# Optimization experiments

Measured on AMD Instinct MI355X. Metric: run time of the kernel, lower is better.

## Reference

```python
import jax, jax.numpy as jnp
import numpy as np

H = 512
S = 65  # 64 board cells + appended constant 1


def _heads(y, wk, wq, wv):
    # y: [H, S]; wk/wq/wv: [3, H, H] -> atts: [3, S, H]
    def one(wk_i, wq_i, wv_i):
        k = wk_i @ y            # [H, S]
        q = wq_i @ y            # [H, S]
        v = wv_i @ y            # [H, S]
        sm = jax.nn.softmax(k.T @ q, axis=1)  # [S, S], softmax over dim=1
        return sm @ v.T         # [S, H]
    return jax.vmap(one)(wk, wq, wv)


def setup_inputs() -> dict:
    key = jax.random.key(0)
    ks = jax.random.split(key, 10)
    r = lambda k, s: jax.random.normal(k, s, dtype=jnp.float32)
    return {
        "inputs": r(ks[0], (1, 64)),
        "embedding": r(ks[1], (H, S)),
        "wq": r(ks[2], (3, 3, H, H)),
        "wk": r(ks[3], (3, 3, H, H)),
        "wv": r(ks[4], (3, 3, H, H)),
        "linear1": r(ks[5], (3 * H, H)),
        "linear2": r(ks[6], (3 * H, H)),
        "linear3": r(ks[7], (3 * H, 2 * H)),
        "linear4": r(ks[8], (2 * H, H)),
        "linear5": r(ks[9], (H, 64)),
    }


def reference(inputs, embedding, wq, wk, wv, linear1, linear2, linear3, linear4, linear5):
    x = jnp.concatenate([inputs[0], jnp.ones((1,), inputs.dtype)])  # [S]
    y = embedding * x  # [H, S] (broadcast over rows)

    # Layer 1 (3 heads)
    a1 = _heads(y, wk[0], wq[0], wv[0])  # [3, S, H]
    y = jax.nn.relu(jnp.concatenate([a1[0], a1[1], a1[2]], axis=1) @ linear1).T  # [H, S]

    # Layer 2 -- NOTE: original code cats att11, att12, att23 (a bug we preserve)
    a2 = _heads(y, wk[1], wq[1], wv[1])
    y = jax.nn.relu(jnp.concatenate([a1[0], a1[1], a2[2]], axis=1) @ linear2).T  # [H, S]

    # Layer 3 -- NOTE: original code cats att11, att12, att33 (preserved)
    a3 = _heads(y, wk[2], wq[2], wv[2])
    y = jax.nn.relu(jnp.concatenate([a1[0], a1[1], a3[2]], axis=1) @ linear3)[64]  # [2H]

    # dropout p=0.1 -> identity in eval mode
    y = jnp.tanh(y @ linear4)  # [H]
    score = y @ linear5        # [64]
    return score[None, :]      # [1, 64]
```

## Files before the change

kernel.cpp:

```cpp
#include <hip/hip_runtime.h>
#include <hip/hip_bf16.h>
#include <math.h>

#define H 512
#define S 65
#define SP 80
#define HS (H * S)
#define PHS (H * SP)
#define KS3 24
#define KS4 16


__global__ void scale_embed_kernel(const float* __restrict__ inp,
                                   const float* __restrict__ emb,
                                   float* __restrict__ yT) {
    int i = blockIdx.x * blockDim.x + threadIdx.x;
    if (i < PHS) {
        int s = i / H;
        int h = i % H;
        float v = 0.f;
        if (s < S) {
            float x = (s == 64) ? 1.0f : inp[s];
            v = emb[h * S + s] * x;
        }
        yT[i] = v;
    }
}

__global__ void __launch_bounds__(256, 2)
kqv_gemm_tiled(const float* __restrict__ wq,
               const float* __restrict__ wk,
               const float* __restrict__ wv,
               int layer, int head0,
               const float* __restrict__ yT,
               float* __restrict__ part) {
    int slot  = blockIdx.z;
    int which = blockIdx.y;
    int mat = layer * 3 + head0 + slot;
    const float* W = (which == 0 ? wk : (which == 1 ? wq : wv)) + (size_t)mat * H * H;

    int n0   = (blockIdx.x & 7) * 64;
    int kidx = blockIdx.x >> 3;

    __shared__ float Wt[64 * 64];
    __shared__ float As[SP * 64];

    int t  = threadIdx.x;
    int nq = t & 15;
    int g  = t >> 4;

    float4 acc[5];
#pragma unroll
    for (int r = 0; r < 5; ++r) acc[r] = make_float4(0.f, 0.f, 0.f, 0.f);

    for (int ch = 0; ch < 4; ++ch) {
        int kc0 = kidx * 256 + ch * 64;
#pragma unroll
        for (int c = 0; c < 4; ++c) {
            int f = c * 256 + t;
            int wn  = f >> 4;
            int kf4 = f & 15;
            float4 w4 = *(const float4*)(W + (size_t)(n0 + wn) * H + kc0 + 4 * kf4);
            int sw = ((wn >> 2) ^ (kf4 & 7));
            int base = (4 * kf4) * 64 + 4 * sw + (wn & 3);
            Wt[base      ] = w4.x;
            Wt[base +  64] = w4.y;
            Wt[base + 128] = w4.z;
            Wt[base + 192] = w4.w;
        }
#pragma unroll
        for (int c = 0; c < 5; ++c) {
            int f = c * 256 + t;
            int as  = f >> 4;
            int kf4 = f & 15;
            *(float4*)(&As[as * 64 + 4 * kf4]) =
                *(const float4*)(yT + (size_t)as * H + kc0 + 4 * kf4);
        }
        __syncthreads();

#pragma unroll
        for (int k4 = 0; k4 < 16; ++k4) {
            int swc = 4 * (nq ^ (k4 & 7));
            float4 w0 = *(const float4*)(&Wt[(4 * k4 + 0) * 64 + swc]);
            float4 w1 = *(const float4*)(&Wt[(4 * k4 + 1) * 64 + swc]);
            float4 w2 = *(const float4*)(&Wt[(4 * k4 + 2) * 64 + swc]);
            float4 w3 = *(const float4*)(&Wt[(4 * k4 + 3) * 64 + swc]);
#pragma unroll
            for (int r = 0; r < 5; ++r) {
                float4 a = *(const float4*)(&As[(g + 16 * r) * 64 + 4 * k4]);
                acc[r].x = fmaf(a.x, w0.x, acc[r].x);
                acc[r].y = fmaf(a.x, w0.y, acc[r].y);
                acc[r].z = fmaf(a.x, w0.z, acc[r].z);
                acc[r].w = fmaf(a.x, w0.w, acc[r].w);
                acc[r].x = fmaf(a.y, w1.x, acc[r].x);
                acc[r].y = fmaf(a.y, w1.y, acc[r].y);
                acc[r].z = fmaf(a.y, w1.z, acc[r].z);
                acc[r].w = fmaf(a.y, w1.w, acc[r].w);
                acc[r].x = fmaf(a.z, w2.x, acc[r].x);
                acc[r].y = fmaf(a.z, w2.y, acc[r].y);
                acc[r].z = fmaf(a.z, w2.z, acc[r].z);
                acc[r].w = fmaf(a.z, w2.w, acc[r].w);
                acc[r].x = fmaf(a.w, w3.x, acc[r].x);
                acc[r].y = fmaf(a.w, w3.y, acc[r].y);
                acc[r].z = fmaf(a.w, w3.z, acc[r].z);
                acc[r].w = fmaf(a.w, w3.w, acc[r].w);
            }
        }
        __syncthreads();
    }

    float* P = part + (size_t)((slot * 3 + which) * 2 + kidx) * PHS;
#pragma unroll
    for (int r = 0; r < 5; ++r) {
        *(float4*)(P + (size_t)(g + 16 * r) * H + n0 + 4 * nq) = acc[r];
    }
}

__device__ __forceinline__ float score_part(const float* __restrict__ Q0,
                                            const float* __restrict__ Q1,
                                            const float* __restrict__ ka,
                                            int b, int t) {
    const float4* q0 = (const float4*)(Q0 + (size_t)b * H) + t * 32;
    const float4* q1 = (const float4*)(Q1 + (size_t)b * H) + t * 32;
    const float4* kl = (const float4*)ka + t * 32;
    float4 c0 = {0,0,0,0}, c1 = {0,0,0,0};
#pragma unroll
    for (int u = 0; u < 32; u += 2) {
        float4 qa = q0[u], qb = q1[u], k0 = kl[u];
        float4 qc = q0[u+1], qd = q1[u+1], k1 = kl[u+1];
        c0.x = fmaf(k0.x, qa.x + qb.x, c0.x);
        c0.y = fmaf(k0.y, qa.y + qb.y, c0.y);
        c0.z = fmaf(k0.z, qa.z + qb.z, c0.z);
        c0.w = fmaf(k0.w, qa.w + qb.w, c0.w);
        c1.x = fmaf(k1.x, qc.x + qd.x, c1.x);
        c1.y = fmaf(k1.y, qc.y + qd.y, c1.y);
        c1.z = fmaf(k1.z, qc.z + qd.z, c1.z);
        c1.w = fmaf(k1.w, qc.w + qd.w, c1.w);
    }
    return ((c0.x + c0.y) + (c0.z + c0.w)) + ((c1.x + c1.y) + (c1.z + c1.w));
}

__global__ void attn_kernel(const float* __restrict__ kqvp,
                            float* __restrict__ att) {
    int a = blockIdx.x;
    int slot = blockIdx.y;
    int tid = threadIdx.x;

    const float* base = kqvp + (size_t)slot * 6 * PHS;
    const float* K0 = base;
    const float* K1 = base + PHS;
    const float* Q0 = base + 2 * (size_t)PHS;
    const float* Q1 = base + 3 * (size_t)PHS;
    const float* V0 = base + 4 * (size_t)PHS;
    const float* V1 = base + 5 * (size_t)PHS;
    float* ao = att + (size_t)slot * PHS + (size_t)a * H;

    __shared__ float ka[H];
    __shared__ float sp[4 * 65];
    __shared__ float smv[S];
    __shared__ float p[S];

    ka[tid]       = K0[(size_t)a * H + tid]       + K1[(size_t)a * H + tid];
    ka[tid + 256] = K0[(size_t)a * H + tid + 256] + K1[(size_t)a * H + tid + 256];
    __syncthreads();

    {
        int b = tid & 63;
        int t = tid >> 6;
        sp[t * 65 + b] = score_part(Q0, Q1, ka, b, t);
        if (tid < 4) sp[tid * 65 + 64] = score_part(Q0, Q1, ka, 64, tid);
    }
    __syncthreads();

    if (tid < S) {
        smv[tid] = (sp[tid] + sp[65 + tid]) + (sp[130 + tid] + sp[195 + tid]);
    }
    __syncthreads();

    float maxv = -INFINITY;
    for (int i = 0; i < S; ++i) maxv = fmaxf(maxv, smv[i]);
    float sum = 0.0f;
    for (int i = 0; i < S; ++i) sum += expf(smv[i] - maxv);
    float inv = 1.0f / sum;
    if (tid < S) p[tid] = expf(smv[tid] - maxv) * inv;
    __syncthreads();

#pragma unroll
    for (int rep = 0; rep < 2; ++rep) {
        int hh = tid + rep * 256;
        float a0 = 0.f, a1 = 0.f;
#pragma unroll 4
        for (int b = 0; b < 64; b += 2) {
            a0 = fmaf(p[b    ], V0[(size_t)(b    ) * H + hh] + V1[(size_t)(b    ) * H + hh], a0);
            a1 = fmaf(p[b + 1], V0[(size_t)(b + 1) * H + hh] + V1[(size_t)(b + 1) * H + hh], a1);
        }
        a0 = fmaf(p[64], V0[(size_t)64 * H + hh] + V1[(size_t)64 * H + hh], a0);
        ao[hh] = a0 + a1;
    }
}

__device__ __forceinline__ void lin_gemm_dev(const float* __restrict__ A01,
                                             const float* __restrict__ A2,
                                             const float* __restrict__ L,
                                             float* __restrict__ Pbase,
                                             int ntile, int kidx, int kbase,
                                             int tid,
                                             float* __restrict__ Bs,
                                             float* __restrict__ As) {
    int n0 = ntile * 64;
    int nq = tid & 15;
    int g  = tid >> 4;

    float4 acc[5];
#pragma unroll
    for (int r = 0; r < 5; ++r) acc[r] = make_float4(0.f, 0.f, 0.f, 0.f);

#pragma unroll
    for (int ch = 0; ch < 2; ++ch) {
        int kg = kbase + kidx * 128 + ch * 64;
        int head = kg >> 9;
        const float* Asrc = (head < 2) ? (A01 + (size_t)head * PHS) : A2;
        int col0 = kg & 511;

#pragma unroll
        for (int c = 0; c < 4; ++c) {
            int f = c * 256 + tid;
            int kk  = f >> 4;
            int hf4 = f & 15;
            *(float4*)(&Bs[kk * 64 + 4 * hf4]) =
                *(const float4*)(L + (size_t)(kg + kk) * H + n0 + 4 * hf4);
        }
#pragma unroll
        for (int c = 0; c < 5; ++c) {
            int f = c * 256 + tid;
            int as  = f >> 4;
            int kf4 = f & 15;
            *(float4*)(&As[as * 68 + 4 * kf4]) =
                *(const float4*)(Asrc + (size_t)as * H + col0 + 4 * kf4);
        }
        __syncthreads();

#pragma unroll
        for (int k4 = 0; k4 < 16; ++k4) {
            float4 w0 = *(const float4*)(&Bs[(4 * k4 + 0) * 64 + 4 * nq]);
            float4 w1 = *(const float4*)(&Bs[(4 * k4 + 1) * 64 + 4 * nq]);
            float4 w2 = *(const float4*)(&Bs[(4 * k4 + 2) * 64 + 4 * nq]);
            float4 w3 = *(const float4*)(&Bs[(4 * k4 + 3) * 64 + 4 * nq]);
#pragma unroll
            for (int r = 0; r < 5; ++r) {
                float4 a = *(const float4*)(&As[(g + 16 * r) * 68 + 4 * k4]);
                acc[r].x = fmaf(a.x, w0.x, acc[r].x);
                acc[r].y = fmaf(a.x, w0.y, acc[r].y);
                acc[r].z = fmaf(a.x, w0.z, acc[r].z);
                acc[r].w = fmaf(a.x, w0.w, acc[r].w);
                acc[r].x = fmaf(a.y, w1.x, acc[r].x);
                acc[r].y = fmaf(a.y, w1.y, acc[r].y);
                acc[r].z = fmaf(a.y, w1.z, acc[r].z);
                acc[r].w = fmaf(a.y, w1.w, acc[r].w);
                acc[r].x = fmaf(a.z, w2.x, acc[r].x);
                acc[r].y = fmaf(a.z, w2.y, acc[r].y);
                acc[r].z = fmaf(a.z, w2.z, acc[r].z);
                acc[r].w = fmaf(a.z, w2.w, acc[r].w);
                acc[r].x = fmaf(a.w, w3.x, acc[r].x);
                acc[r].y = fmaf(a.w, w3.y, acc[r].y);
                acc[r].z = fmaf(a.w, w3.z, acc[r].z);
                acc[r].w = fmaf(a.w, w3.w, acc[r].w);
            }
        }
        __syncthreads();
    }

    float* P = Pbase + (size_t)kidx * PHS;
#pragma unroll
    for (int r = 0; r < 5; ++r) {
        *(float4*)(P + (size_t)(g + 16 * r) * H + n0 + 4 * nq) = acc[r];
    }
}

__global__ void __launch_bounds__(256, 1)
lin1plus_kernel(const float* __restrict__ att1,
                const float* __restrict__ lin1,
                const float* __restrict__ lin3,
                float* __restrict__ plin1,
                float* __restrict__ tpart) {
    __shared__ float Bs[64 * 64];
    __shared__ float As[SP * 68];
    int bx = blockIdx.x;
    int tid = threadIdx.x;

    if (bx < 96) {
        lin_gemm_dev(att1, att1 + 2 * (size_t)PHS, lin1, plin1,
                     bx & 7, bx >> 3, 0, tid, Bs, As);
    } else {
        int idx = bx - 96;
        int j2 = (idx & 3) * 256 + tid;
        int ks = idx >> 2;
        const float* row = att1 + (size_t)(ks >> 3) * PHS + (size_t)64 * H;
        int j0 = (ks & 7) * 64;
        int jbase = ks * 64;
        float a0 = 0.f, a1 = 0.f, a2 = 0.f, a3 = 0.f;
        for (int j = 0; j < 64; j += 4) {
            a0 = fmaf(row[j0 + j + 0], lin3[(size_t)(jbase + j + 0) * 1024 + j2], a0);
            a1 = fmaf(row[j0 + j + 1], lin3[(size_t)(jbase + j + 1) * 1024 + j2], a1);
            a2 = fmaf(row[j0 + j + 2], lin3[(size_t)(jbase + j + 2) * 1024 + j2], a2);
            a3 = fmaf(row[j0 + j + 3], lin3[(size_t)(jbase + j + 3) * 1024 + j2], a3);
        }
        tpart[ks * 1024 + j2] = (a0 + a1) + (a2 + a3);
    }
}

__global__ void __launch_bounds__(256, 1)
lin2ab_kernel(const float* __restrict__ att1,
              const float* __restrict__ lin2,
              float* __restrict__ plin2) {
    __shared__ float Bs[64 * 64];
    __shared__ float As[SP * 68];
    int bx = blockIdx.x;
    lin_gemm_dev(att1, att1, lin2, plin2, bx & 7, bx >> 3, 0,
                 threadIdx.x, Bs, As);
}

__global__ void __launch_bounds__(256, 1)
lin2c_kernel(const float* __restrict__ att2,
             const float* __restrict__ lin2,
             float* __restrict__ plin2) {
    __shared__ float Bs[64 * 64];
    __shared__ float As[SP * 68];
    int bx = blockIdx.x;
    lin_gemm_dev(att2, att2, lin2, plin2 + 8 * (size_t)PHS,
                 bx & 7, bx >> 3, 1024, threadIdx.x, Bs, As);
}

__global__ void combine12_relu_kernel(const float* __restrict__ part,
                                      float* __restrict__ yT) {
    int i = blockIdx.x * 256 + threadIdx.x;
    float s = 0.f;
#pragma unroll
    for (int p = 0; p < 12; ++p) s += part[(size_t)p * PHS + i];
    yT[i] = fmaxf(s, 0.0f);
}

__global__ void attn3_lin3c_kernel(const float* __restrict__ kqvp,
                                   const float* __restrict__ lin3,
                                   float* __restrict__ tpart) {
    int tid = threadIdx.x;
    int ks  = 16 + blockIdx.y;
    int j2  = blockIdx.x * 256 + tid;
    int j0  = (ks & 7) * 64;

    const float* K0 = kqvp;
    const float* K1 = kqvp + PHS;
    const float* Q0 = kqvp + 2 * (size_t)PHS;
    const float* Q1 = kqvp + 3 * (size_t)PHS;
    const float* V0 = kqvp + 4 * (size_t)PHS;
    const float* V1 = kqvp + 5 * (size_t)PHS;

    __shared__ float ka[H];
    __shared__ float sp[4 * 65];
    __shared__ float smv[S];
    __shared__ float p[S];
    __shared__ float att_s[64];

    ka[tid]       = K0[(size_t)64 * H + tid]       + K1[(size_t)64 * H + tid];
    ka[tid + 256] = K0[(size_t)64 * H + tid + 256] + K1[(size_t)64 * H + tid + 256];
    __syncthreads();

    {
        int b = tid & 63;
        int t = tid >> 6;
        sp[t * 65 + b] = score_part(Q0, Q1, ka, b, t);
        if (tid < 4) sp[tid * 65 + 64] = score_part(Q0, Q1, ka, 64, tid);
    }
    __syncthreads();

    if (tid < S) {
        smv[tid] = (sp[tid] + sp[65 + tid]) + (sp[130 + tid] + sp[195 + tid]);
    }
    __syncthreads();

    float maxv = -INFINITY;
    for (int i = 0; i < S; ++i) maxv = fmaxf(maxv, smv[i]);
    float sum = 0.0f;
    for (int i = 0; i < S; ++i) sum += expf(smv[i] - maxv);
    float inv = 1.0f / sum;
    if (tid < S) p[tid] = expf(smv[tid] - maxv) * inv;
    __syncthreads();

    if (tid < 64) {
        int hh = j0 + tid;
        float a0 = 0.f, a1 = 0.f;
#pragma unroll 4
        for (int b = 0; b < 64; b += 2) {
            a0 = fmaf(p[b    ], V0[(size_t)(b    ) * H + hh] + V1[(size_t)(b    ) * H + hh], a0);
            a1 = fmaf(p[b + 1], V0[(size_t)(b + 1) * H + hh] + V1[(size_t)(b + 1) * H + hh], a1);
        }
        a0 = fmaf(p[64], V0[(size_t)64 * H + hh] + V1[(size_t)64 * H + hh], a0);
        att_s[tid] = a0 + a1;
    }
    __syncthreads();

    int jbase = ks * 64;
    float a0 = 0.f, a1 = 0.f, a2 = 0.f, a3 = 0.f;
    for (int j = 0; j < 64; j += 4) {
        a0 = fmaf(att_s[j + 0], lin3[(size_t)(jbase + j + 0) * 1024 + j2], a0);
        a1 = fmaf(att_s[j + 1], lin3[(size_t)(jbase + j + 1) * 1024 + j2], a1);
        a2 = fmaf(att_s[j + 2], lin3[(size_t)(jbase + j + 2) * 1024 + j2], a2);
        a3 = fmaf(att_s[j + 3], lin3[(size_t)(jbase + j + 3) * 1024 + j2], a3);
    }
    tpart[ks * 1024 + j2] = (a0 + a1) + (a2 + a3);
}

__global__ void lin4_partial_kernel(const float* __restrict__ tpart,
                                    const float* __restrict__ lin4,
                                    float* __restrict__ upart) {
    __shared__ float tl[64];
    int hh = blockIdx.x * 256 + threadIdx.x;
    int ks = blockIdx.y;
    int j2base = ks * 64;

    if (threadIdx.x < 64) {
        int j2 = j2base + threadIdx.x;
        float s = 0.f;
#pragma unroll
        for (int p = 0; p < KS3; ++p) s += tpart[p * 1024 + j2];
        tl[threadIdx.x] = fmaxf(s, 0.f);
    }
    __syncthreads();

    float a0 = 0.f, a1 = 0.f, a2 = 0.f, a3 = 0.f;
    for (int j = 0; j < 64; j += 4) {
        a0 = fmaf(tl[j + 0], lin4[(size_t)(j2base + j + 0) * H + hh], a0);
        a1 = fmaf(tl[j + 1], lin4[(size_t)(j2base + j + 1) * H + hh], a1);
        a2 = fmaf(tl[j + 2], lin4[(size_t)(j2base + j + 2) * H + hh], a2);
        a3 = fmaf(tl[j + 3], lin4[(size_t)(j2base + j + 3) * H + hh], a3);
    }
    upart[ks * H + hh] = (a0 + a1) + (a2 + a3);
}

__global__ void final_out_kernel(const float* __restrict__ upart,
                                 const float* __restrict__ lin5,
                                 float* __restrict__ out) {
    __shared__ float u[H];
    __shared__ float pr[8][64];
    int tid = threadIdx.x;

    {
        float s = 0.f;
#pragma unroll
        for (int p = 0; p < KS4; ++p) s += upart[p * H + tid];
        u[tid] = tanhf(s);
    }
    __syncthreads();

    int o  = tid & 63;
    int sl = tid >> 6;
    float acc = 0.f;
    int h0 = sl * 64;
#pragma unroll 8
    for (int j = 0; j < 64; ++j) {
        acc = fmaf(u[h0 + j], lin5[(h0 + j) * 64 + o], acc);
    }
    pr[sl][o] = acc;
    __syncthreads();

    if (tid < 64) {
        float s = 0.f;
#pragma unroll
        for (int p = 0; p < 8; ++p) s += pr[p][tid];
        out[tid] = s;
    }
}

extern "C" void kernel_launch(void* const* d_in, const int* in_sizes, int n_in,
                              void* d_out, int out_size, void* d_ws, size_t ws_size,
                              hipStream_t stream) {
    const float* inputs  = (const float*)d_in[0];
    const float* emb     = (const float*)d_in[1];
    const float* wq      = (const float*)d_in[2];
    const float* wk      = (const float*)d_in[3];
    const float* wv      = (const float*)d_in[4];
    const float* linear1 = (const float*)d_in[5];
    const float* linear2 = (const float*)d_in[6];
    const float* linear3 = (const float*)d_in[7];
    const float* linear4 = (const float*)d_in[8];
    const float* linear5 = (const float*)d_in[9];
    float* out = (float*)d_out;

    float* ws    = (float*)d_ws;
    float* y     = ws;
    float* kqvp  = y     + PHS;
    float* att1  = kqvp  + 18 * PHS;
    float* att2  = att1  + 3 * PHS;
    float* plin1 = att2  + PHS;
    float* plin2 = plin1 + 12 * PHS;
    float* tpart = plin2 + 12 * PHS;
    float* upart = tpart + KS3 * 1024;

    const int nb  = HS / 256;
    const int nbp = PHS / 256;

    scale_embed_kernel<<<nbp, 256, 0, stream>>>(inputs, emb, y);

    kqv_gemm_tiled<<<dim3(16, 3, 3), 256, 0, stream>>>(wq, wk, wv, 0, 0, y, kqvp);
    attn_kernel<<<dim3(S, 3), 256, 0, stream>>>(kqvp, att1);
    lin1plus_kernel<<<160, 256, 0, stream>>>(att1, linear1, linear3, plin1, tpart);
    lin2ab_kernel<<<64, 256, 0, stream>>>(att1, linear2, plin2);
    combine12_relu_kernel<<<nb, 256, 0, stream>>>(plin1, y);

    kqv_gemm_tiled<<<dim3(16, 3, 1), 256, 0, stream>>>(wq, wk, wv, 1, 2, y, kqvp);
    attn_kernel<<<dim3(S, 1), 256, 0, stream>>>(kqvp, att2);
    lin2c_kernel<<<32, 256, 0, stream>>>(att2, linear2, plin2);
    combine12_relu_kernel<<<nb, 256, 0, stream>>>(plin2, y);

    kqv_gemm_tiled<<<dim3(16, 3, 1), 256, 0, stream>>>(wq, wk, wv, 2, 2, y, kqvp);
    attn3_lin3c_kernel<<<dim3(4, 8), 256, 0, stream>>>(kqvp, linear3, tpart);

    lin4_partial_kernel<<<dim3(2, KS4), 256, 0, stream>>>(tpart, linear4, upart);
    final_out_kernel<<<1, 512, 0, stream>>>(upart, linear5, out);
}
```

Baseline: 304.6 us.

## Fuse partial-sum combine and ReLU into QKV loads; merge linear kernels

The two linear-layer GEMM launches are merged into one large kernel, and the tiled shared-memory GEMM is replaced by a simple per-output dot product with 256-wide K splits, which gives 6 partials instead of 12. The separate combine-plus-ReLU kernels are removed: the templated QKV GEMM now sums the 6 partials and applies ReLU while it loads its activations. This cuts launch count and intermediate traffic. The cost is that the untiled dot product gives up shared-memory reuse, so every weight element is re-read from cache once per sequence row, and the QKV kernel's occupancy hint drops to one block.

```diff
diff --git a/kernel.cpp b/kernel.cpp
--- a/kernel.cpp
+++ b/kernel.cpp
@@ -27,16 +27,17 @@
     }
 }
 
-__global__ void __launch_bounds__(256, 2)
+template <int COMBINE>
+__global__ void __launch_bounds__(256, 1)
 kqv_gemm_tiled(const float* __restrict__ wq,
                const float* __restrict__ wk,
                const float* __restrict__ wv,
-               int layer, int head0,
-               const float* __restrict__ yT,
+               int mat0,
+               const float* __restrict__ src,
                float* __restrict__ part) {
     int slot  = blockIdx.z;
     int which = blockIdx.y;
-    int mat = layer * 3 + head0 + slot;
+    int mat = mat0 + slot;
     const float* W = (which == 0 ? wk : (which == 1 ? wq : wv)) + (size_t)mat * H * H;
 
     int n0   = (blockIdx.x & 7) * 64;
@@ -73,8 +74,21 @@
             int f = c * 256 + t;
             int as  = f >> 4;
             int kf4 = f & 15;
-            *(float4*)(&As[as * 64 + 4 * kf4]) =
-                *(const float4*)(yT + (size_t)as * H + kc0 + 4 * kf4);
+            const float* addr = src + (size_t)as * H + kc0 + 4 * kf4;
+            float4 v;
+            if (COMBINE) {
+                v = make_float4(0.f, 0.f, 0.f, 0.f);
+#pragma unroll
+                for (int p = 0; p < 6; ++p) {
+                    float4 u = *(const float4*)(addr + (size_t)p * PHS);
+                    v.x += u.x; v.y += u.y; v.z += u.z; v.w += u.w;
+                }
+                v.x = fmaxf(v.x, 0.f); v.y = fmaxf(v.y, 0.f);
+                v.z = fmaxf(v.z, 0.f); v.w = fmaxf(v.w, 0.f);
+            } else {
+                v = *(const float4*)addr;
+            }
+            *(float4*)(&As[as * 64 + 4 * kf4]) = v;
         }
         __syncthreads();
 
@@ -199,100 +213,48 @@
     }
 }
 
-__device__ __forceinline__ void lin_gemm_dev(const float* __restrict__ A01,
-                                             const float* __restrict__ A2,
-                                             const float* __restrict__ L,
-                                             float* __restrict__ Pbase,
-                                             int ntile, int kidx, int kbase,
-                                             int tid,
-                                             float* __restrict__ Bs,
-                                             float* __restrict__ As) {
-    int n0 = ntile * 64;
-    int nq = tid & 15;
-    int g  = tid >> 4;
-
-    float4 acc[5];
-#pragma unroll
-    for (int r = 0; r < 5; ++r) acc[r] = make_float4(0.f, 0.f, 0.f, 0.f);
-
-#pragma unroll
-    for (int ch = 0; ch < 2; ++ch) {
-        int kg = kbase + kidx * 128 + ch * 64;
-        int head = kg >> 9;
-        const float* Asrc = (head < 2) ? (A01 + (size_t)head * PHS) : A2;
-        int col0 = kg & 511;
-
-#pragma unroll
-        for (int c = 0; c < 4; ++c) {
-            int f = c * 256 + tid;
-            int kk  = f >> 4;
-            int hf4 = f & 15;
-            *(float4*)(&Bs[kk * 64 + 4 * hf4]) =
-                *(const float4*)(L + (size_t)(kg + kk) * H + n0 + 4 * hf4);
-        }
-#pragma unroll
-        for (int c = 0; c < 5; ++c) {
-            int f = c * 256 + tid;
-            int as  = f >> 4;
-            int kf4 = f & 15;
-            *(float4*)(&As[as * 68 + 4 * kf4]) =
-                *(const float4*)(Asrc + (size_t)as * H + col0 + 4 * kf4);
-        }
-        __syncthreads();
-
-#pragma unroll
-        for (int k4 = 0; k4 < 16; ++k4) {
-            float4 w0 = *(const float4*)(&Bs[(4 * k4 + 0) * 64 + 4 * nq]);
-            float4 w1 = *(const float4*)(&Bs[(4 * k4 + 1) * 64 + 4 * nq]);
-            float4 w2 = *(const float4*)(&Bs[(4 * k4 + 2) * 64 + 4 * nq]);
-            float4 w3 = *(const float4*)(&Bs[(4 * k4 + 3) * 64 + 4 * nq]);
-#pragma unroll
-            for (int r = 0; r < 5; ++r) {
-                float4 a = *(const float4*)(&As[(g + 16 * r) * 68 + 4 * k4]);
-                acc[r].x = fmaf(a.x, w0.x, acc[r].x);
-                acc[r].y = fmaf(a.x, w0.y, acc[r].y);
-                acc[r].z = fmaf(a.x, w0.z, acc[r].z);
-                acc[r].w = fmaf(a.x, w0.w, acc[r].w);
-                acc[r].x = fmaf(a.y, w1.x, acc[r].x);
-                acc[r].y = fmaf(a.y, w1.y, acc[r].y);
-                acc[r].z = fmaf(a.y, w1.z, acc[r].z);
-                acc[r].w = fmaf(a.y, w1.w, acc[r].w);
-                acc[r].x = fmaf(a.z, w2.x, acc[r].x);
-                acc[r].y = fmaf(a.z, w2.y, acc[r].y);
-                acc[r].z = fmaf(a.z, w2.z, acc[r].z);
-                acc[r].w = fmaf(a.z, w2.w, acc[r].w);
-                acc[r].x = fmaf(a.w, w3.x, acc[r].x);
-                acc[r].y = fmaf(a.w, w3.y, acc[r].y);
-                acc[r].z = fmaf(a.w, w3.z, acc[r].z);
-                acc[r].w = fmaf(a.w, w3.w, acc[r].w);
-            }
-        }
-        __syncthreads();
-    }
-
-    float* P = Pbase + (size_t)kidx * PHS;
-#pragma unroll
-    for (int r = 0; r < 5; ++r) {
-        *(float4*)(P + (size_t)(g + 16 * r) * H + n0 + 4 * nq) = acc[r];
-    }
-}
-
-__global__ void __launch_bounds__(256, 1)
-lin1plus_kernel(const float* __restrict__ att1,
-                const float* __restrict__ lin1,
-                const float* __restrict__ lin3,
-                float* __restrict__ plin1,
-                float* __restrict__ tpart) {
-    __shared__ float Bs[64 * 64];
-    __shared__ float As[SP * 68];
+__global__ void mega_lin_kernel(const float* __restrict__ att1,
+                                const float* __restrict__ lin1,
+                                const float* __restrict__ lin2,
+                                const float* __restrict__ lin3,
+                                float* __restrict__ plin1,
+                                float* __restrict__ plin2,
+                                float* __restrict__ tpart) {
     int bx = blockIdx.x;
     int tid = threadIdx.x;
 
-    if (bx < 96) {
-        lin_gemm_dev(att1, att1 + 2 * (size_t)PHS, lin1, plin1,
-                     bx & 7, bx >> 3, 0, tid, Bs, As);
+    if (bx < 1300) {
+        const float* att;
+        const float* L;
+        float* dst;
+        int x, seg;
+        if (bx < 780) {
+            seg = bx / 130; x = bx - seg * 130;
+            att = att1 + (size_t)(seg >> 1) * PHS;
+            L   = lin1 + (size_t)(seg * 256) * H;
+            dst = plin1 + (size_t)seg * PHS;
+        } else {
+            int b2 = bx - 780;
+            seg = b2 / 130; x = b2 - seg * 130;
+            att = att1 + (size_t)(seg >> 1) * PHS;
+            L   = lin2 + (size_t)(seg * 256) * H;
+            dst = plin2 + (size_t)seg * PHS;
+        }
+        int i = x * 256 + tid;
+        int s = i / H;
+        int h = i % H;
+        const float* row = att + (size_t)s * H + (seg & 1) * 256;
+        const float* Lh = L + h;
+        float a0 = 0.f, a1 = 0.f, a2 = 0.f, a3 = 0.f;
+        for (int j = 0; j < 256; j += 4) {
+            a0 = fmaf(row[j + 0], Lh[(size_t)(j + 0) * H], a0);
+            a1 = fmaf(row[j + 1], Lh[(size_t)(j + 1) * H], a1);
+            a2 = fmaf(row[j + 2], Lh[(size_t)(j + 2) * H], a2);
+            a3 = fmaf(row[j + 3], Lh[(size_t)(j + 3) * H], a3);
+        }
+        dst[(size_t)s * H + h] = (a0 + a1) + (a2 + a3);
     } else {
-        int idx = bx - 96;
+        int idx = bx - 1300;
         int j2 = (idx & 3) * 256 + tid;
         int ks = idx >> 2;
         const float* row = att1 + (size_t)(ks >> 3) * PHS + (size_t)64 * H;
@@ -309,35 +271,23 @@
     }
 }
 
-__global__ void __launch_bounds__(256, 1)
-lin2ab_kernel(const float* __restrict__ att1,
-              const float* __restrict__ lin2,
-              float* __restrict__ plin2) {
-    __shared__ float Bs[64 * 64];
-    __shared__ float As[SP * 68];
-    int bx = blockIdx.x;
-    lin_gemm_dev(att1, att1, lin2, plin2, bx & 7, bx >> 3, 0,
-                 threadIdx.x, Bs, As);
-}
-
-__global__ void __launch_bounds__(256, 1)
-lin2c_kernel(const float* __restrict__ att2,
-             const float* __restrict__ lin2,
-             float* __restrict__ plin2) {
-    __shared__ float Bs[64 * 64];
-    __shared__ float As[SP * 68];
-    int bx = blockIdx.x;
-    lin_gemm_dev(att2, att2, lin2, plin2 + 8 * (size_t)PHS,
-                 bx & 7, bx >> 3, 1024, threadIdx.x, Bs, As);
-}
-
-__global__ void combine12_relu_kernel(const float* __restrict__ part,
-                                      float* __restrict__ yT) {
+__global__ void lin2c_kernel(const float* __restrict__ att2,
+                             const float* __restrict__ lin2,
+                             float* __restrict__ plin2) {
+    int seg = 4 + blockIdx.y;
     int i = blockIdx.x * 256 + threadIdx.x;
-    float s = 0.f;
-#pragma unroll
-    for (int p = 0; p < 12; ++p) s += part[(size_t)p * PHS + i];
-    yT[i] = fmaxf(s, 0.0f);
+    int s = i / H;
+    int h = i % H;
+    const float* row = att2 + (size_t)s * H + (seg & 1) * 256;
+    const float* Lh = lin2 + (size_t)(seg * 256) * H + h;
+    float a0 = 0.f, a1 = 0.f, a2 = 0.f, a3 = 0.f;
+    for (int j = 0; j < 256; j += 4) {
+        a0 = fmaf(row[j + 0], Lh[(size_t)(j + 0) * H], a0);
+        a1 = fmaf(row[j + 1], Lh[(size_t)(j + 1) * H], a1);
+        a2 = fmaf(row[j + 2], Lh[(size_t)(j + 2) * H], a2);
+        a3 = fmaf(row[j + 3], Lh[(size_t)(j + 3) * H], a3);
+    }
+    plin2[(size_t)seg * PHS + (size_t)s * H + h] = (a0 + a1) + (a2 + a3);
 }
 
 __global__ void attn3_lin3c_kernel(const float* __restrict__ kqvp,
@@ -492,27 +442,24 @@
     float* att1  = kqvp  + 18 * PHS;
     float* att2  = att1  + 3 * PHS;
     float* plin1 = att2  + PHS;
-    float* plin2 = plin1 + 12 * PHS;
-    float* tpart = plin2 + 12 * PHS;
+    float* plin2 = plin1 + 6 * PHS;
+    float* tpart = plin2 + 6 * PHS;
     float* upart = tpart + KS3 * 1024;
 
-    const int nb  = HS / 256;
     const int nbp = PHS / 256;
 
     scale_embed_kernel<<<nbp, 256, 0, stream>>>(inputs, emb, y);
 
-    kqv_gemm_tiled<<<dim3(16, 3, 3), 256, 0, stream>>>(wq, wk, wv, 0, 0, y, kqvp);
+    kqv_gemm_tiled<0><<<dim3(16, 3, 3), 256, 0, stream>>>(wq, wk, wv, 0, y, kqvp);
     attn_kernel<<<dim3(S, 3), 256, 0, stream>>>(kqvp, att1);
-    lin1plus_kernel<<<160, 256, 0, stream>>>(att1, linear1, linear3, plin1, tpart);
-    lin2ab_kernel<<<64, 256, 0, stream>>>(att1, linear2, plin2);
-    combine12_relu_kernel<<<nb, 256, 0, stream>>>(plin1, y);
-
-    kqv_gemm_tiled<<<dim3(16, 3, 1), 256, 0, stream>>>(wq, wk, wv, 1, 2, y, kqvp);
+    mega_lin_kernel<<<1364, 256, 0, stream>>>(att1, linear1, linear2, linear3,
+                                              plin1, plin2, tpart);
+
+    kqv_gemm_tiled<1><<<dim3(16, 3, 1), 256, 0, stream>>>(wq, wk, wv, 5, plin1, kqvp);
     attn_kernel<<<dim3(S, 1), 256, 0, stream>>>(kqvp, att2);
-    lin2c_kernel<<<32, 256, 0, stream>>>(att2, linear2, plin2);
-    combine12_relu_kernel<<<nb, 256, 0, stream>>>(plin2, y);
-
-    kqv_gemm_tiled<<<dim3(16, 3, 1), 256, 0, stream>>>(wq, wk, wv, 2, 2, y, kqvp);
+    lin2c_kernel<<<dim3(130, 2), 256, 0, stream>>>(att2, linear2, plin2);
+
+    kqv_gemm_tiled<1><<<dim3(16, 3, 1), 256, 0, stream>>>(wq, wk, wv, 8, plin2, kqvp);
     attn3_lin3c_kernel<<<dim3(4, 8), 256, 0, stream>>>(kqvp, linear3, tpart);
 
     lin4_partial_kernel<<<dim3(2, KS4), 256, 0, stream>>>(tpart, linear4, upart);
```

New measurement: 260.4 us. 14.5% less time.
